# Kernel optimization log

Measured on AMD Instinct MI355X. Metric: run time of the kernel, lower is better.

## Reference

```python
import jax, jax.numpy as jnp
import numpy as np

B, T, E, HD, K, V = 128, 512, 128, 128, 20, 30000  # HD = hidden per direction


def _lstm_dir(x, Wih, Whh, b, reverse):
    # x: [T, B, D]; Wih: [4H, D]; Whh: [4H, H]; b: [4H] (b_ih + b_hh combined)
    if reverse:
        x = x[::-1]
    bsz = x.shape[1]
    xW = jnp.einsum('tbd,gd->tbg', x, Wih) + b  # [T, B, 4H] precompute input proj
    h0 = jnp.zeros((bsz, HD), x.dtype)
    c0 = jnp.zeros((bsz, HD), x.dtype)

    def step(carry, xw):
        h, c = carry
        z = xw + h @ Whh.T
        i, f, g, o = jnp.split(z, 4, axis=-1)  # PyTorch gate order i,f,g,o
        c = jax.nn.sigmoid(f) * c + jax.nn.sigmoid(i) * jnp.tanh(g)
        h = jax.nn.sigmoid(o) * jnp.tanh(c)
        return (h, c), h

    _, hs = jax.lax.scan(step, (h0, c0), xW)
    if reverse:
        hs = hs[::-1]
    return hs


def _bilstm_layer(x, Wih, Whh, b):
    # Wih/Whh: [2, 4H, D]/[2, 4H, H]; b: [2, 4H]
    hf = _lstm_dir(x, Wih[0], Whh[0], b[0], False)
    hb = _lstm_dir(x, Wih[1], Whh[1], b[1], True)
    return jnp.concatenate([hf, hb], axis=-1)  # [T, B, 2H]


def _crf_nll(emissions, tags, trans, start, end):
    # emissions: [B, T, K]; tags: [B, T]; full (all-ones) mask, reduction='mean'
    bsz = emissions.shape[0]
    em_tm = jnp.swapaxes(emissions, 0, 1)  # [T, B, K]
    tags_tm = tags.T                       # [T, B]
    bidx = jnp.arange(bsz)

    # --- numerator: path score ---
    score0 = start[tags_tm[0]] + em_tm[0][bidx, tags_tm[0]]

    def num_step(s, inp):
        em_t, tg_prev, tg_t = inp
        return s + trans[tg_prev, tg_t] + em_t[bidx, tg_t], None

    score, _ = jax.lax.scan(num_step, score0, (em_tm[1:], tags_tm[:-1], tags_tm[1:]))
    score = score + end[tags_tm[-1]]

    # --- denominator: forward algorithm (log partition) ---
    alpha0 = start[None, :] + em_tm[0]  # [B, K]

    def den_step(a, em_t):
        # a[b,i] + trans[i,j] + em_t[b,j] -> logsumexp over i
        a = jax.nn.logsumexp(a[:, :, None] + trans[None], axis=1) + em_t
        return a, None

    alpha, _ = jax.lax.scan(den_step, alpha0, em_tm[1:])
    logZ = jax.nn.logsumexp(alpha + end[None, :], axis=1)

    return -jnp.mean(score - logZ)


def setup_inputs() -> dict:
    key = jax.random.key(0)
    ks = jax.random.split(key, 16)
    u = lambda k, shape, s: jax.random.uniform(k, shape, jnp.float32, -s, s)
    kk = 1.0 / np.sqrt(HD)
    embed = jax.random.normal(ks[0], (V, E), jnp.float32) * 0.1
    embed = embed.at[0].set(0.0)  # padding_idx=0
    inp = {
        'sentences': jax.random.randint(ks[1], (B, T), 1, V),  # no pad tokens -> full mask
        'tags': jax.random.randint(ks[2], (B, T), 0, K),
        'lengths': jnp.full((B,), T, dtype=jnp.int64 if jax.config.jax_enable_x64 else jnp.int32),
        'embed': embed,
        'Wih0': u(ks[3], (2, 4 * HD, E), kk),
        'Whh0': u(ks[4], (2, 4 * HD, HD), kk),
        'b0': u(ks[5], (2, 4 * HD), kk),
        'Wih1': u(ks[6], (2, 4 * HD, 2 * HD), kk),
        'Whh1': u(ks[7], (2, 4 * HD, HD), kk),
        'b1': u(ks[8], (2, 4 * HD), kk),
        'Wout': u(ks[9], (K, 2 * HD), 1.0 / np.sqrt(2 * HD)),
        'bout': u(ks[10], (K,), 1.0 / np.sqrt(2 * HD)),
        'trans': u(ks[11], (K, K), 0.1),
        'start': u(ks[12], (K,), 0.1),
        'end': u(ks[13], (K,), 0.1),
    }
    return inp


def reference(sentences, tags, lengths, embed, Wih0, Whh0, b0, Wih1, Whh1, b1, Wout, bout, trans, start, end):
    # all lengths == T, so pack/pad is identity (eval-mode: no dropout)
    x = embed[sentences]                 # [B, T, E]
    x = jnp.swapaxes(x, 0, 1)            # [T, B, E] time-major for scan
    x = _bilstm_layer(x, Wih0, Whh0, b0)  # [T, B, 2H]
    x = _bilstm_layer(x, Wih1, Whh1, b1)  # [T, B, 2H]
    emissions = jnp.einsum('tbh,kh->tbk', x, Wout) + bout  # [T, B, K]
    emissions = jnp.swapaxes(emissions, 0, 1)              # [B, T, K]
    return _crf_nll(emissions, tags, trans, start, end)
```

## Files before the change

kernel.cpp:

```cpp
#include <hip/hip_runtime.h>
#include <hip/hip_bf16.h>
#include <cstddef>

typedef unsigned short u16;
typedef unsigned int u32;
typedef short bf16x8 __attribute__((ext_vector_type(8)));
typedef unsigned short u16x8 __attribute__((ext_vector_type(8)));
typedef float f32x4 __attribute__((ext_vector_type(4)));
typedef int i32x4 __attribute__((ext_vector_type(4)));
typedef int i32x8 __attribute__((ext_vector_type(8)));

constexpr int CB = 128;
constexpr int CT = 512;
constexpr int CE = 128;
constexpr int CK = 20;

constexpr size_t OFF_FLAG   = 0;
constexpr size_t OFF_WIH0   = 256;
constexpr size_t OFF_WHH0   = OFF_WIH0 + 262144;
constexpr size_t OFF_WIH1   = OFF_WHH0 + 262144;
constexpr size_t OFF_WHH1   = OFF_WIH1 + 524288;
constexpr size_t OFF_WOUT   = OFF_WHH1 + 262144;
constexpr size_t OFF_B0     = OFF_WOUT + 10240;
constexpr size_t OFF_B1     = OFF_B0 + 4096;
constexpr size_t OFF_BOUT   = OFF_B1 + 4096;
constexpr size_t OFF_TRANS  = OFF_BOUT + 256;
constexpr size_t OFF_START  = OFF_TRANS + 1792;
constexpr size_t OFF_END    = OFF_START + 256;
constexpr size_t OFF_PART   = OFF_END + 256;
constexpr size_t OFF_WHH0F8 = OFF_PART + 256;
constexpr size_t OFF_WHH1F8 = OFF_WHH0F8 + 131072;
constexpr size_t OFF_X0     = 2097152;
constexpr size_t OFF_H0     = OFF_X0 + 16777216;
constexpr size_t OFF_H1     = OFF_H0 + 33554432;
constexpr size_t OFF_EM     = OFF_H1 + 33554432;
constexpr size_t OFF_Z      = OFF_EM + 5242880;
constexpr size_t WS_NEED    = OFF_Z + 134217728;

__device__ __forceinline__ float b2f(u16 u) {
    union { u32 i; float f; } v; v.i = ((u32)u) << 16; return v.f;
}
__device__ __forceinline__ u16 f2b(float f) {
    union { float f; u32 i; } v; v.f = f;
    u32 r = v.i + 0x7FFFu + ((v.i >> 16) & 1u);
    return (u16)(r >> 16);
}
__device__ __forceinline__ float ldin(const void* p, long i, int bf) {
    return bf ? b2f(((const u16*)p)[i]) : ((const float*)p)[i];
}
__device__ __forceinline__ float sigm(float x) { return 1.0f / (1.0f + __expf(-x)); }
__device__ __forceinline__ float tanh_f(float x) { return 2.0f / (1.0f + __expf(-2.0f * x)) - 1.0f; }

__device__ __forceinline__ void gload_lds16(const void* g, void* l) {
    __builtin_amdgcn_global_load_lds(
        (const __attribute__((address_space(1))) void*)g,
        (__attribute__((address_space(3))) void*)l, 16, 0, 0);
}

__global__ void sniff_k(const unsigned char* __restrict__ traw, int* __restrict__ flag) {
    int lane = threadIdx.x;
    int votes = 0;
    for (int w = lane; w < 200; w += 64) {
        unsigned char b1 = traw[w * 4 + 1];
        unsigned char e = b1 & 0x7F;
        if (e >= 0x20 && e <= 0x3E) votes++;
    }
    #pragma unroll
    for (int off = 32; off; off >>= 1) votes += __shfl_xor(votes, off);
    if (lane == 0) *flag = (votes > 120) ? 1 : 0;
}

__global__ __launch_bounds__(256) void prep_k(
    const void* wih0, const void* whh0, const void* b0,
    const void* wih1, const void* whh1, const void* b1,
    const void* wout, const void* bout, const void* trans,
    const void* start, const void* end, unsigned char* ws)
{
    const int bf = *(const int*)(ws + OFF_FLAG);
    long tid = (long)blockIdx.x * 256 + threadIdx.x;
    u16* wih0b = (u16*)(ws + OFF_WIH0);
    u16* whh0b = (u16*)(ws + OFF_WHH0);
    u16* wih1b = (u16*)(ws + OFF_WIH1);
    u16* whh1b = (u16*)(ws + OFF_WHH1);
    u16* woutb = (u16*)(ws + OFF_WOUT);
    float* b0f   = (float*)(ws + OFF_B0);
    float* b1f   = (float*)(ws + OFF_B1);
    float* boutf = (float*)(ws + OFF_BOUT);
    float* trf   = (float*)(ws + OFF_TRANS);
    float* stf   = (float*)(ws + OFF_START);
    float* enf   = (float*)(ws + OFF_END);

    if (tid < 131072) { wih0b[tid] = f2b(ldin(wih0, tid, bf)); return; } tid -= 131072;
    if (tid < 131072) { whh0b[tid] = f2b(ldin(whh0, tid, bf)); return; } tid -= 131072;
    if (tid < 1024)   { b0f[tid]   = ldin(b0, tid, bf);        return; } tid -= 1024;
    if (tid < 262144) { wih1b[tid] = f2b(ldin(wih1, tid, bf)); return; } tid -= 262144;
    if (tid < 131072) { whh1b[tid] = f2b(ldin(whh1, tid, bf)); return; } tid -= 131072;
    if (tid < 1024)   { b1f[tid]   = ldin(b1, tid, bf);        return; } tid -= 1024;
    if (tid < 5120)   { woutb[tid] = f2b(ldin(wout, tid, bf)); return; } tid -= 5120;
    if (tid < 20)     { boutf[tid] = ldin(bout, tid, bf);      return; } tid -= 20;
    if (tid < 400)    { trf[tid]   = ldin(trans, tid, bf);     return; } tid -= 400;
    if (tid < 20)     { stf[tid]   = ldin(start, tid, bf);     return; } tid -= 20;
    if (tid < 20)     { enf[tid]   = ldin(end, tid, bf);       return; } tid -= 20;
    if (tid < 65536) {
        const float v0 = ldin(whh0, tid * 2, bf) * 8.0f;
        const float v1 = ldin(whh0, tid * 2 + 1, bf) * 8.0f;
        const u32 pk = __builtin_amdgcn_cvt_pk_fp8_f32(v0, v1, 0, false);
        ((u16*)(ws + OFF_WHH0F8))[tid] = (u16)(pk & 0xFFFF);
        return;
    } tid -= 65536;
    if (tid < 65536) {
        const float v0 = ldin(whh1, tid * 2, bf) * 8.0f;
        const float v1 = ldin(whh1, tid * 2 + 1, bf) * 8.0f;
        const u32 pk = __builtin_amdgcn_cvt_pk_fp8_f32(v0, v1, 0, false);
        ((u16*)(ws + OFF_WHH1F8))[tid] = (u16)(pk & 0xFFFF);
        return;
    }
}

__global__ __launch_bounds__(256) void gather_k(const void* __restrict__ embed,
                                                const int* __restrict__ sent,
                                                unsigned char* __restrict__ ws)
{
    const int bf = *(const int*)(ws + OFF_FLAG);
    u16* x0 = (u16*)(ws + OFF_X0);
    int tid = blockIdx.x * 256 + threadIdx.x;
    int m = tid >> 4, ch = tid & 15;
    int t = m >> 7, b = m & 127;
    int s = sent[b * CT + t];
    long src = (long)s * CE + ch * 8;
    u16x8 o;
    if (bf) {
        o = *(const u16x8*)((const u16*)embed + src);
    } else {
        const float* ef = (const float*)embed + src;
        f32x4 lo = *(const f32x4*)ef;
        f32x4 hi = *(const f32x4*)(ef + 4);
        o[0]=f2b(lo[0]); o[1]=f2b(lo[1]); o[2]=f2b(lo[2]); o[3]=f2b(lo[3]);
        o[4]=f2b(hi[0]); o[5]=f2b(hi[1]); o[6]=f2b(hi[2]); o[7]=f2b(hi[3]);
    }
    *(u16x8*)(x0 + (long)m * CE + ch * 8) = o;
}

template<int KD>
__global__ __launch_bounds__(256) void gemm_k(const u16* __restrict__ A,
                                              const u16* __restrict__ Bw,
                                              const float* __restrict__ bias,
                                              u16* __restrict__ Zp)
{
    const int bm = blockIdx.x >> 3, bn = blockIdx.x & 7;
    const long m0 = (long)bm * 128;
    const int n0 = bn * 128;
    const int tid = threadIdx.x, lane = tid & 63, wave = tid >> 6;
    const int wm = wave >> 1, wn = wave & 1;
    const int lr = lane & 15, kg = (lane >> 4) * 8;

    __shared__ __align__(16) u16 At[128][32];
    __shared__ __align__(16) u16 Bt[128][32];
    __shared__ __align__(16) u16 cho[128][136];
    __shared__ float bsm[128];
    if (tid < 128) bsm[tid] = bias[n0 + tid];

    f32x4 acc[4][4];
    #pragma unroll
    for (int i = 0; i < 4; ++i)
        #pragma unroll
        for (int j = 0; j < 4; ++j) acc[i][j] = (f32x4){0.f, 0.f, 0.f, 0.f};

    const int srow = tid >> 2, scol = (tid & 3) * 8;
    char* atb = (char*)&At[0][0] + wave * 1024;
    char* btb = (char*)&Bt[0][0] + wave * 1024;
    for (int kk = 0; kk < KD; kk += 32) {
        __syncthreads();
        gload_lds16(A + (m0 + srow) * KD + kk + scol, atb);
        gload_lds16(A + (m0 + srow + 64) * KD + kk + scol, atb + 4096);
        gload_lds16(Bw + (long)(n0 + srow) * KD + kk + scol, btb);
        gload_lds16(Bw + (long)(n0 + srow + 64) * KD + kk + scol, btb + 4096);
        __syncthreads();
        bf16x8 af[4], bfv[4];
        #pragma unroll
        for (int mt = 0; mt < 4; ++mt)
            af[mt] = *(const bf16x8*)&At[wm * 64 + mt * 16 + lr][kg];
        #pragma unroll
        for (int nt = 0; nt < 4; ++nt)
            bfv[nt] = *(const bf16x8*)&Bt[wn * 64 + nt * 16 + lr][kg];
        #pragma unroll
        for (int mt = 0; mt < 4; ++mt)
            #pragma unroll
            for (int nt = 0; nt < 4; ++nt)
                acc[mt][nt] = __builtin_amdgcn_mfma_f32_16x16x32_bf16(
                    af[mt], bfv[nt], acc[mt][nt], 0, 0, 0);
    }

    __syncthreads();
    const int rr0 = (lane >> 4) * 4;
    #pragma unroll
    for (int mt = 0; mt < 4; ++mt)
        #pragma unroll
        for (int nt = 0; nt < 4; ++nt) {
            const int colw = wn * 64 + nt * 16 + lr;
            const int pc = (colw >> 5) * 32 + ((colw & 15) << 1) + ((colw >> 4) & 1);
            const float bv = bsm[colw];
            #pragma unroll
            for (int r = 0; r < 4; ++r)
                cho[wm * 64 + mt * 16 + rr0 + r][pc] = f2b(acc[mt][nt][r] + bv);
        }
    __syncthreads();
    const int brow = tid >> 1, hf = tid & 1;
    const int dd = n0 >> 9, gt = (n0 >> 7) & 3;
    const int t = bm;
    const int sz = dd ? (CT - 1 - t) : t;
    u16* dst = Zp + ((long)(brow * 2 + dd) * CT + sz) * 512 + gt * 128 + hf * 64;
    const u16* srcl = &cho[brow][hf * 64];
    #pragma unroll
    for (int p = 0; p < 8; ++p)
        *(u16x8*)(dst + p * 8) = *(const u16x8*)(srcl + p * 8);
}

__global__ __launch_bounds__(256, 1) void scan_k(const u16* __restrict__ Zp,
                                                 const unsigned char* __restrict__ Whh8,
                                                 u16* __restrict__ hout)
{
    const int b = blockIdx.x & 127, d = blockIdx.x >> 7;
    const int tid = threadIdx.x;
    const int lane = tid & 63;
    const int wave = tid >> 6;
    const int lr = lane & 15;
    const int kb8 = (lane >> 4) * 32;
    const int uhalf = (lane >> 4) & 1;
    const int rowm = wave * 32 + (lane & 31);

    i32x8 bfrag[4][2];
    #pragma unroll
    for (int gt = 0; gt < 4; ++gt)
        #pragma unroll
        for (int uu = 0; uu < 2; ++uu) {
            const unsigned char* wb = Whh8 +
                ((long)(d * 512 + gt * 128 + wave * 32 + uu * 16 + lr) << 7) + kb8;
            const i32x4 lo = *(const i32x4*)wb;
            const i32x4 hi = *(const i32x4*)(wb + 16);
            bfrag[gt][uu] = (i32x8){lo[0], lo[1], lo[2], lo[3], hi[0], hi[1], hi[2], hi[3]};
        }

    __shared__ __align__(16) unsigned char hbuf8[2 * 128];

    const u16* zseq = Zp + (long)(b * 2 + d) * CT * 512;
    const u32* zw0 = (const u32*)zseq + wave * 16 + lr;

    u32 zR[16][4];
    #pragma unroll
    for (int s = 0; s < 16; ++s) {
        #pragma unroll
        for (int g = 0; g < 4; ++g)
            zR[s][g] = zw0[s * 256 + g * 64];
    }
    const u32* znext = zw0 + 16 * 256;

    if (tid < 128) { hbuf8[tid] = 0; hbuf8[128 + tid] = 0; }
    asm volatile("s_waitcnt lgkmcnt(0)\n\ts_barrier" ::: "memory");

    float cst = 0.f;
    u16* hp = hout + ((long)(d ? (CT - 1) : 0) * CB + b) * 256 + d * 128 + rowm;
    const long hstep = (long)(d ? -1 : 1) * (CB * 256);

    for (int grp = 0; grp < 32; ++grp) {
        const bool more = grp < 31;
        #pragma unroll
        for (int slot = 0; slot < 16; ++slot) {
            const u32 zl0 = zR[slot][0], zl1 = zR[slot][1];
            const u32 zl2 = zR[slot][2], zl3 = zR[slot][3];
            if (more) {
                zR[slot][0] = znext[slot * 256];
                zR[slot][1] = znext[slot * 256 + 64];
                zR[slot][2] = znext[slot * 256 + 128];
                zR[slot][3] = znext[slot * 256 + 192];
            }

            const unsigned char* hbp = hbuf8 + (slot & 1) * 128 + kb8;
            const i32x4 hlo = *(const i32x4*)hbp;
            const i32x4 hhi = *(const i32x4*)(hbp + 16);
            const i32x8 av = (i32x8){hlo[0], hlo[1], hlo[2], hlo[3],
                                     hhi[0], hhi[1], hhi[2], hhi[3]};

            f32x4 acc[4][2];
            #pragma unroll
            for (int gt = 0; gt < 4; ++gt) {
                acc[gt][0] = (f32x4){0.f, 0.f, 0.f, 0.f};
                acc[gt][1] = (f32x4){0.f, 0.f, 0.f, 0.f};
            }
            #pragma unroll
            for (int gt = 0; gt < 4; ++gt) {
                acc[gt][0] = __builtin_amdgcn_mfma_scale_f32_16x16x128_f8f6f4(
                    av, bfrag[gt][0], acc[gt][0], 0, 0,
                    0, 0x7F7F7F7F, 0, 0x7F7F7F7F);
                acc[gt][1] = __builtin_amdgcn_mfma_scale_f32_16x16x128_f8f6f4(
                    av, bfrag[gt][1], acc[gt][1], 0, 0,
                    0, 0x7F7F7F7F, 0, 0x7F7F7F7F);
            }

            const u32 zlw[4] = {zl0, zl1, zl2, zl3};
            float pg[4];
            #pragma unroll
            for (int gt = 0; gt < 4; ++gt) {
                union { u32 i; float f; } zz;
                zz.i = uhalf ? (zlw[gt] & 0xFFFF0000u) : (zlw[gt] << 16);
                const float sv = uhalf ? acc[gt][1][0] : acc[gt][0][0];
                pg[gt] = fmaf(sv, 0.125f, zz.f);
            }
            const float iv = sigm(pg[0]);
            const float fv = sigm(pg[1]);
            const float gg = tanh_f(pg[2]);
            const float ov = sigm(pg[3]);
            cst = fmaf(fv, cst, iv * gg);
            const float h = ov * tanh_f(cst);

            if (lane < 32) {
                const u32 pk = __builtin_amdgcn_cvt_pk_fp8_f32(h, h, 0, false);
                hbuf8[((slot + 1) & 1) * 128 + rowm] = (unsigned char)(pk & 0xFF);
                *hp = f2b(h);
            }
            hp += hstep;
            asm volatile("s_waitcnt lgkmcnt(0)\n\ts_barrier" ::: "memory");
        }
        znext += 4096;
    }
}

__global__ __launch_bounds__(256) void emis_k(const u16* __restrict__ h1,
                                              const u16* __restrict__ woutb,
                                              const float* __restrict__ boutf,
                                              float* __restrict__ em)
{
    __shared__ __align__(16) float wsm[CK * 256];
    for (int i = threadIdx.x; i < CK * 256; i += 256) wsm[i] = b2f(woutb[i]);
    __syncthreads();
    const long m = (long)blockIdx.x * 256 + threadIdx.x;
    const u16* hrow = h1 + m * 256;
    float acc[CK];
    #pragma unroll
    for (int n = 0; n < CK; ++n) acc[n] = boutf[n];
    for (int k8 = 0; k8 < 32; ++k8) {
        u16x8 u = *(const u16x8*)(hrow + k8 * 8);
        float hv[8];
        #pragma unroll
        for (int j = 0; j < 8; ++j) hv[j] = b2f(u[j]);
        #pragma unroll
        for (int n = 0; n < CK; ++n) {
            const f32x4 w0 = *(const f32x4*)&wsm[n * 256 + k8 * 8];
            const f32x4 w1 = *(const f32x4*)&wsm[n * 256 + k8 * 8 + 4];
            acc[n] = fmaf(hv[0], w0[0], acc[n]); acc[n] = fmaf(hv[1], w0[1], acc[n]);
            acc[n] = fmaf(hv[2], w0[2], acc[n]); acc[n] = fmaf(hv[3], w0[3], acc[n]);
            acc[n] = fmaf(hv[4], w1[0], acc[n]); acc[n] = fmaf(hv[5], w1[1], acc[n]);
            acc[n] = fmaf(hv[6], w1[2], acc[n]); acc[n] = fmaf(hv[7], w1[3], acc[n]);
        }
    }
    float* emrow = em + m * CK;
    #pragma unroll
    for (int n = 0; n < CK; ++n) emrow[n] = acc[n];
}

__global__ void crf_k(const float* __restrict__ em, const int* __restrict__ tags,
                      const float* __restrict__ trf, const float* __restrict__ stf,
                      const float* __restrict__ enf, float* __restrict__ partial)
{
    const int lane = threadIdx.x;
    if (blockIdx.x < 64) {
        const int j = lane & 31, half = lane >> 5;
        const int b = blockIdx.x * 2 + half;
        const bool act = j < CK;
        float tcol[CK];
        #pragma unroll
        for (int i = 0; i < CK; ++i) tcol[i] = act ? __expf(trf[i * CK + j]) : 0.f;
        float p = act ? __expf(stf[j] + em[(long)b * CK + j]) : 0.f;
        float L = 0.f;
        float emn = act ? em[((long)1 * CB + b) * CK + j] : 0.f;
        for (int t = 1; t < CT; ++t) {
            const float emv = emn;
            if (t + 1 < CT)
                emn = act ? em[((long)(t + 1) * CB + b) * CK + j] : 0.f;
            float pi[CK];
            #pragma unroll
            for (int i = 0; i < CK; ++i) pi[i] = __shfl(p, i, 32);
            float a0 = 0.f, a1 = 0.f, a2 = 0.f, a3 = 0.f;
            #pragma unroll
            for (int i = 0; i < CK; i += 4) {
                a0 = fmaf(pi[i], tcol[i], a0);
                a1 = fmaf(pi[i + 1], tcol[i + 1], a1);
                a2 = fmaf(pi[i + 2], tcol[i + 2], a2);
                a3 = fmaf(pi[i + 3], tcol[i + 3], a3);
            }
            p = ((a0 + a1) + (a2 + a3)) * __expf(emv);
            if ((t & 7) == 0) {
                float sum = act ? p : 0.f;
                #pragma unroll
                for (int off = 16; off; off >>= 1) sum += __shfl_xor(sum, off, 32);
                L += __logf(sum);
                p *= (1.0f / sum);
            }
        }
        float vv = act ? (__logf(p) + L + enf[j]) : -1e30f;
        float mx = vv;
        #pragma unroll
        for (int off = 16; off; off >>= 1) mx = fmaxf(mx, __shfl_xor(mx, off, 32));
        float ex = act ? __expf(vv - mx) : 0.f;
        #pragma unroll
        for (int off = 16; off; off >>= 1) ex += __shfl_xor(ex, off, 32);
        if (j == 0) partial[b] = mx + __logf(ex);
    } else {
        const int b = blockIdx.x - 64;
        float sc = 0.f;
        for (int t = lane; t < CT; t += 64) {
            const int tg = tags[b * CT + t];
            sc += em[((long)t * CB + b) * CK + tg];
            if (t >= 1) sc += trf[tags[b * CT + t - 1] * CK + tg];
        }
        #pragma unroll
        for (int off = 32; off; off >>= 1) sc += __shfl_xor(sc, off);
        if (lane == 0)
            partial[128 + b] = sc + stf[tags[b * CT]] + enf[tags[b * CT + CT - 1]];
    }
}

__global__ void fin_k(const float* __restrict__ partial, void* __restrict__ out,
                      const unsigned char* __restrict__ ws)
{
    const int bf = *(const int*)(ws + OFF_FLAG);
    const int lane = threadIdx.x;
    float v = (partial[lane] - partial[128 + lane]) + (partial[lane + 64] - partial[192 + lane]);
    #pragma unroll
    for (int off = 32; off; off >>= 1) v += __shfl_xor(v, off);
    if (lane == 0) {
        const float mean = v / 128.f;
        if (bf) ((u16*)out)[0] = f2b(mean);
        else    ((float*)out)[0] = mean;
    }
}

extern "C" void kernel_launch(void* const* d_in, const int* in_sizes, int n_in,
                              void* d_out, int out_size, void* d_ws, size_t ws_size,
                              hipStream_t stream) {
    (void)in_sizes; (void)n_in; (void)out_size;
    if (ws_size < WS_NEED) return;
    unsigned char* ws = (unsigned char*)d_ws;

    const void* sent  = d_in[0];
    const void* tags  = d_in[1];
    const void* embed = d_in[3];

    u16* x0  = (u16*)(ws + OFF_X0);
    u16* h0  = (u16*)(ws + OFF_H0);
    u16* h1  = (u16*)(ws + OFF_H1);
    u16* Zb  = (u16*)(ws + OFF_Z);
    float* em = (float*)(ws + OFF_EM);
    float* part = (float*)(ws + OFF_PART);

    sniff_k<<<1, 64, 0, stream>>>((const unsigned char*)d_in[12], (int*)(ws + OFF_FLAG));
    prep_k<<<3102, 256, 0, stream>>>(d_in[4], d_in[5], d_in[6], d_in[7], d_in[8],
                                     d_in[9], d_in[10], d_in[11], d_in[12], d_in[13],
                                     d_in[14], ws);
    gather_k<<<4096, 256, 0, stream>>>(embed, (const int*)sent, ws);
    gemm_k<128><<<4096, 256, 0, stream>>>(x0, (const u16*)(ws + OFF_WIH0),
                                          (const float*)(ws + OFF_B0), Zb);
    scan_k<<<256, 256, 0, stream>>>(Zb, (const unsigned char*)(ws + OFF_WHH0F8), h0);
    gemm_k<256><<<4096, 256, 0, stream>>>(h0, (const u16*)(ws + OFF_WIH1),
                                          (const float*)(ws + OFF_B1), Zb);
    scan_k<<<256, 256, 0, stream>>>(Zb, (const unsigned char*)(ws + OFF_WHH1F8), h1);
    emis_k<<<256, 256, 0, stream>>>(h1, (const u16*)(ws + OFF_WOUT),
                                    (const float*)(ws + OFF_BOUT), em);
    crf_k<<<192, 64, 0, stream>>>(em, (const int*)tags,
                                  (const float*)(ws + OFF_TRANS),
                                  (const float*)(ws + OFF_START),
                                  (const float*)(ws + OFF_END), part);
    fin_k<<<1, 64, 0, stream>>>(part, d_out, ws);
}
```

Before: 888.4 us.

## Process two batch sequences per LSTM scan block to halve grid size

Each scan block now advances two batch sequences at once: lanes 0-31 handle one sequence and lanes 32-63 the other. Each wave issues MFMAs against both fp8 hidden-state buffers while sharing the register-resident Whh fragments. The grid drops from 256 to 128 blocks, and the Z prefetch depth is halved to make room for the extra accumulators. The aim is to use the lanes that previously sat idle and to avoid a second wave of blocks on the CUs. The cost is twice the MFMA and LDS work per step on the serial critical path.

```diff
diff --git a/kernel.cpp b/kernel.cpp
--- a/kernel.cpp
+++ b/kernel.cpp
@@ -220,13 +220,17 @@
                                                  const unsigned char* __restrict__ Whh8,
                                                  u16* __restrict__ hout)
 {
-    const int b = blockIdx.x & 127, d = blockIdx.x >> 7;
+    const int d = blockIdx.x >> 6;
+    const int b0 = (blockIdx.x & 63) * 2;
     const int tid = threadIdx.x;
     const int lane = tid & 63;
     const int wave = tid >> 6;
     const int lr = lane & 15;
-    const int kb8 = (lane >> 4) * 32;
+    const int kb8 = ((lane >> 4) & 1) * 32 + (lane >> 5) * 64;
+    const int kgrp = (lane >> 4) * 32;
     const int uhalf = (lane >> 4) & 1;
+    const int myseq = lane >> 5;
+    const int myb = b0 + myseq;
     const int rowm = wave * 32 + (lane & 31);
 
     i32x8 bfrag[4][2];
@@ -235,37 +239,40 @@
         #pragma unroll
         for (int uu = 0; uu < 2; ++uu) {
             const unsigned char* wb = Whh8 +
-                ((long)(d * 512 + gt * 128 + wave * 32 + uu * 16 + lr) << 7) + kb8;
+                ((long)(d * 512 + gt * 128 + wave * 32 + uu * 16 + lr) << 7) + kgrp;
             const i32x4 lo = *(const i32x4*)wb;
             const i32x4 hi = *(const i32x4*)(wb + 16);
             bfrag[gt][uu] = (i32x8){lo[0], lo[1], lo[2], lo[3], hi[0], hi[1], hi[2], hi[3]};
         }
 
-    __shared__ __align__(16) unsigned char hbuf8[2 * 128];
-
-    const u16* zseq = Zp + (long)(b * 2 + d) * CT * 512;
+    __shared__ __align__(16) unsigned char hbuf8[2][2][128];
+
+    const u16* zseq = Zp + (long)(myb * 2 + d) * CT * 512;
     const u32* zw0 = (const u32*)zseq + wave * 16 + lr;
 
-    u32 zR[16][4];
-    #pragma unroll
-    for (int s = 0; s < 16; ++s) {
+    u32 zR[8][4];
+    #pragma unroll
+    for (int s = 0; s < 8; ++s) {
         #pragma unroll
         for (int g = 0; g < 4; ++g)
             zR[s][g] = zw0[s * 256 + g * 64];
     }
-    const u32* znext = zw0 + 16 * 256;
-
-    if (tid < 128) { hbuf8[tid] = 0; hbuf8[128 + tid] = 0; }
+    const u32* znext = zw0 + 8 * 256;
+
+    if (tid < 128) {
+        hbuf8[0][0][tid] = 0; hbuf8[0][1][tid] = 0;
+        hbuf8[1][0][tid] = 0; hbuf8[1][1][tid] = 0;
+    }
     asm volatile("s_waitcnt lgkmcnt(0)\n\ts_barrier" ::: "memory");
 
     float cst = 0.f;
-    u16* hp = hout + ((long)(d ? (CT - 1) : 0) * CB + b) * 256 + d * 128 + rowm;
+    u16* hp = hout + ((long)(d ? (CT - 1) : 0) * CB + myb) * 256 + d * 128 + rowm;
     const long hstep = (long)(d ? -1 : 1) * (CB * 256);
 
-    for (int grp = 0; grp < 32; ++grp) {
-        const bool more = grp < 31;
-        #pragma unroll
-        for (int slot = 0; slot < 16; ++slot) {
+    for (int grp = 0; grp < 64; ++grp) {
+        const bool more = grp < 63;
+        #pragma unroll
+        for (int slot = 0; slot < 8; ++slot) {
             const u32 zl0 = zR[slot][0], zl1 = zR[slot][1];
             const u32 zl2 = zR[slot][2], zl3 = zR[slot][3];
             if (more) {
@@ -275,26 +282,34 @@
                 zR[slot][3] = znext[slot * 256 + 192];
             }
 
-            const unsigned char* hbp = hbuf8 + (slot & 1) * 128 + kb8;
-            const i32x4 hlo = *(const i32x4*)hbp;
-            const i32x4 hhi = *(const i32x4*)(hbp + 16);
-            const i32x8 av = (i32x8){hlo[0], hlo[1], hlo[2], hlo[3],
-                                     hhi[0], hhi[1], hhi[2], hhi[3]};
-
-            f32x4 acc[4][2];
+            const int par = slot & 1;
+            const unsigned char* hA = &hbuf8[0][par][0] + kgrp;
+            const unsigned char* hB = &hbuf8[1][par][0] + kgrp;
+            const i32x4 al = *(const i32x4*)hA;
+            const i32x4 ah = *(const i32x4*)(hA + 16);
+            const i32x4 bl = *(const i32x4*)hB;
+            const i32x4 bh = *(const i32x4*)(hB + 16);
+            const i32x8 avA = (i32x8){al[0], al[1], al[2], al[3], ah[0], ah[1], ah[2], ah[3]};
+            const i32x8 avB = (i32x8){bl[0], bl[1], bl[2], bl[3], bh[0], bh[1], bh[2], bh[3]};
+
+            f32x4 accA[4][2], accB[4][2];
             #pragma unroll
             for (int gt = 0; gt < 4; ++gt) {
-                acc[gt][0] = (f32x4){0.f, 0.f, 0.f, 0.f};
-                acc[gt][1] = (f32x4){0.f, 0.f, 0.f, 0.f};
+                accA[gt][0] = (f32x4){0.f, 0.f, 0.f, 0.f};
+                accA[gt][1] = (f32x4){0.f, 0.f, 0.f, 0.f};
+                accB[gt][0] = (f32x4){0.f, 0.f, 0.f, 0.f};
+                accB[gt][1] = (f32x4){0.f, 0.f, 0.f, 0.f};
             }
             #pragma unroll
             for (int gt = 0; gt < 4; ++gt) {
-                acc[gt][0] = __builtin_amdgcn_mfma_scale_f32_16x16x128_f8f6f4(
-                    av, bfrag[gt][0], acc[gt][0], 0, 0,
-                    0, 0x7F7F7F7F, 0, 0x7F7F7F7F);
-                acc[gt][1] = __builtin_amdgcn_mfma_scale_f32_16x16x128_f8f6f4(
-                    av, bfrag[gt][1], acc[gt][1], 0, 0,
-                    0, 0x7F7F7F7F, 0, 0x7F7F7F7F);
+                accA[gt][0] = __builtin_amdgcn_mfma_scale_f32_16x16x128_f8f6f4(
+                    avA, bfrag[gt][0], accA[gt][0], 0, 0, 0, 0x7F7F7F7F, 0, 0x7F7F7F7F);
+                accB[gt][0] = __builtin_amdgcn_mfma_scale_f32_16x16x128_f8f6f4(
+                    avB, bfrag[gt][0], accB[gt][0], 0, 0, 0, 0x7F7F7F7F, 0, 0x7F7F7F7F);
+                accA[gt][1] = __builtin_amdgcn_mfma_scale_f32_16x16x128_f8f6f4(
+                    avA, bfrag[gt][1], accA[gt][1], 0, 0, 0, 0x7F7F7F7F, 0, 0x7F7F7F7F);
+                accB[gt][1] = __builtin_amdgcn_mfma_scale_f32_16x16x128_f8f6f4(
+                    avB, bfrag[gt][1], accB[gt][1], 0, 0, 0, 0x7F7F7F7F, 0, 0x7F7F7F7F);
             }
 
             const u32 zlw[4] = {zl0, zl1, zl2, zl3};
@@ -303,7 +318,9 @@
             for (int gt = 0; gt < 4; ++gt) {
                 union { u32 i; float f; } zz;
                 zz.i = uhalf ? (zlw[gt] & 0xFFFF0000u) : (zlw[gt] << 16);
-                const float sv = uhalf ? acc[gt][1][0] : acc[gt][0][0];
+                const float svA = uhalf ? accA[gt][1][0] : accA[gt][0][0];
+                const float svB = uhalf ? accB[gt][1][0] : accB[gt][0][0];
+                const float sv = myseq ? svB : svA;
                 pg[gt] = fmaf(sv, 0.125f, zz.f);
             }
             const float iv = sigm(pg[0]);
@@ -313,15 +330,13 @@
             cst = fmaf(fv, cst, iv * gg);
             const float h = ov * tanh_f(cst);
 
-            if (lane < 32) {
-                const u32 pk = __builtin_amdgcn_cvt_pk_fp8_f32(h, h, 0, false);
-                hbuf8[((slot + 1) & 1) * 128 + rowm] = (unsigned char)(pk & 0xFF);
-                *hp = f2b(h);
-            }
+            const u32 pk = __builtin_amdgcn_cvt_pk_fp8_f32(h, h, 0, false);
+            hbuf8[myseq][par ^ 1][rowm] = (unsigned char)(pk & 0xFF);
+            *hp = f2b(h);
             hp += hstep;
             asm volatile("s_waitcnt lgkmcnt(0)\n\ts_barrier" ::: "memory");
         }
-        znext += 4096;
+        znext += 2048;
     }
 }
 
@@ -460,10 +475,10 @@
     gather_k<<<4096, 256, 0, stream>>>(embed, (const int*)sent, ws);
     gemm_k<128><<<4096, 256, 0, stream>>>(x0, (const u16*)(ws + OFF_WIH0),
                                           (const float*)(ws + OFF_B0), Zb);
-    scan_k<<<256, 256, 0, stream>>>(Zb, (const unsigned char*)(ws + OFF_WHH0F8), h0);
+    scan_k<<<128, 256, 0, stream>>>(Zb, (const unsigned char*)(ws + OFF_WHH0F8), h0);
     gemm_k<256><<<4096, 256, 0, stream>>>(h0, (const u16*)(ws + OFF_WIH1),
                                           (const float*)(ws + OFF_B1), Zb);
-    scan_k<<<256, 256, 0, stream>>>(Zb, (const unsigned char*)(ws + OFF_WHH1F8), h1);
+    scan_k<<<128, 256, 0, stream>>>(Zb, (const unsigned char*)(ws + OFF_WHH1F8), h1);
     emis_k<<<256, 256, 0, stream>>>(h1, (const u16*)(ws + OFF_WOUT),
                                     (const float*)(ws + OFF_BOUT), em);
     crf_k<<<192, 64, 0, stream>>>(em, (const int*)tags,
```

Result: slower. 1.010 ms (+13.7%).
